# Kernel tuning notes

Hardware: AMD Instinct MI355X
Metric: run time of the kernel (lower is better)

The kernel has to match this reference:

```python
import jax, jax.numpy as jnp
import numpy as np

B, T, C, H = 2, 2048, 1024, 16
D = C // H  # head_dim = 64

def setup_inputs() -> dict:
    key = jax.random.key(0)
    k1, k2, k3 = jax.random.split(key, 3)
    x = jax.random.normal(k1, (B, T, C), dtype=jnp.float32)
    W_qkv = jax.random.normal(k2, (C, 3 * C), dtype=jnp.float32) * (C ** -0.5)
    b_qkv = jnp.zeros((3 * C,), dtype=jnp.float32)
    W_proj = jax.random.normal(k3, (C, C), dtype=jnp.float32) * (C ** -0.5)
    b_proj = jnp.zeros((C,), dtype=jnp.float32)
    return {"x": x, "W_qkv": W_qkv, "b_qkv": b_qkv, "W_proj": W_proj, "b_proj": b_proj}

def reference(x, W_qkv, b_qkv, W_proj, b_proj):
    # qkv projection: [B,T,3C]
    qkv = jnp.einsum('btc,cf->btf', x, W_qkv) + b_qkv
    q, k, v = jnp.split(qkv, 3, axis=-1)
    # split heads -> [B,H,T,D]
    q = q.reshape(B, T, H, D).transpose(0, 2, 1, 3)
    k = k.reshape(B, T, H, D).transpose(0, 2, 1, 3)
    v = v.reshape(B, T, H, D).transpose(0, 2, 1, 3)
    scale = 1.0 / jnp.sqrt(jnp.float32(D))
    att = jnp.einsum('bhqd,bhkd->bhqk', q, k) * scale  # [B,H,T,T]
    causal = jnp.tril(jnp.ones((T, T), dtype=bool))
    att = jnp.where(causal[None, None, :, :], att, jnp.float32(-jnp.inf))
    att = jax.nn.softmax(att, axis=-1)
    y = jnp.einsum('bhqk,bhkd->bhqd', att, v)  # [B,H,T,D]
    y = y.transpose(0, 2, 1, 3).reshape(B, T, C)
    return jnp.einsum('btc,cf->btf', y, W_proj) + b_proj
```

## Files before the change

kernel.cpp:

```cpp
#include <hip/hip_runtime.h>
#include <hip/hip_bf16.h>

#define Bq 2
#define Tq 2048
#define Cq 1024
#define Hq 16
#define Dq 64
#define Mq (Bq * Tq)

typedef __bf16 bf16x8 __attribute__((ext_vector_type(8)));
typedef float f32x4 __attribute__((ext_vector_type(4)));
typedef unsigned uint4v __attribute__((ext_vector_type(4)));
typedef unsigned short u16;

static __device__ __forceinline__ u16 f2bf(float f) {
  union { float f; unsigned u; } v; v.f = f;
  return (u16)((v.u + 0x7fffu + ((v.u >> 16) & 1u)) >> 16);
}

static __device__ __forceinline__ unsigned cvt_pk_bf16(float a, float b) {
  unsigned r;
  asm("v_cvt_pk_bf16_f32 %0, %1, %2" : "=v"(r) : "v"(a), "v"(b));
  return r;
}

static __device__ __forceinline__ f32x4 mfma16(bf16x8 a, bf16x8 b, f32x4 c) {
  return __builtin_amdgcn_mfma_f32_16x16x32_bf16(a, b, c, 0, 0, 0);
}

#define GLD16(g, l)                                                   \
  __builtin_amdgcn_global_load_lds(                                   \
      (const __attribute__((address_space(1))) unsigned int*)(g),     \
      (__attribute__((address_space(3))) unsigned int*)(l), 16, 0, 0)

static __device__ __forceinline__ int swz(int col, int row) {
  return (col & 7) + 8 * (((col >> 3) ^ (row >> 3)) & 7);
}

__global__ __launch_bounds__(256) void convert_x(const float* __restrict__ x,
                                                 u16* __restrict__ xb) {
  int i = (blockIdx.x * 256 + threadIdx.x) * 8;
  float4 a = *(const float4*)(x + i);
  float4 b = *(const float4*)(x + i + 4);
  u16 tmp[8];
  tmp[0] = f2bf(a.x); tmp[1] = f2bf(a.y); tmp[2] = f2bf(a.z); tmp[3] = f2bf(a.w);
  tmp[4] = f2bf(b.x); tmp[5] = f2bf(b.y); tmp[6] = f2bf(b.z); tmp[7] = f2bf(b.w);
  *(uint4*)(xb + i) = *(const uint4*)tmp;
}

__global__ __launch_bounds__(256) void transpose_w(const float* __restrict__ W,
                                                   u16* __restrict__ Wt,
                                                   int K, int N) {
  __shared__ __align__(16) u16 Ts[64][72];
  const int k0 = blockIdx.x * 64, n0 = blockIdx.y * 64;
  const int t = threadIdx.x;
  const int r = t >> 2, c0 = (t & 3) * 16;
  const float* src = W + (size_t)(k0 + r) * N + n0 + c0;
  u16 v16[16];
#pragma unroll
  for (int i = 0; i < 4; i++) {
    float4 f = *(const float4*)(src + 4 * i);
    v16[4 * i + 0] = f2bf(f.x); v16[4 * i + 1] = f2bf(f.y);
    v16[4 * i + 2] = f2bf(f.z); v16[4 * i + 3] = f2bf(f.w);
  }
#pragma unroll
  for (int j = 0; j < 16; j++) Ts[c0 + j][r] = v16[j];
  __syncthreads();
  u16* dst = Wt + (size_t)(n0 + r) * K + k0 + c0;
  *(uint4*)dst = *(const uint4*)&Ts[r][c0];
  *(uint4*)(dst + 8) = *(const uint4*)&Ts[r][c0 + 8];
}

__global__ __launch_bounds__(256) void qkv_gemm(
    const u16* __restrict__ A, const u16* __restrict__ Bt,
    const float* __restrict__ bias,
    u16* __restrict__ qw, u16* __restrict__ kw, u16* __restrict__ vw) {
  const int K = 1024;
  __shared__ __align__(16) u16 As[128][32];
  __shared__ __align__(16) u16 Bs[128][32];
  const int m0 = blockIdx.x * 128, n0 = blockIdx.y * 128;
  const int t = threadIdx.x, lane = t & 63, w = t >> 6;
  const int wm = (w >> 1) * 64, wn = (w & 1) * 64;
  const int l15 = lane & 15, l4 = lane >> 4;
  const int lr = lane >> 2, lc = (lane & 3) * 8;
  f32x4 acc[4][4] = {};
  const u16* ga = A + (size_t)(m0 + w * 16 + lr) * K + lc;
  const u16* gb = Bt + (size_t)(n0 + w * 16 + lr) * K + lc;

  for (int kk = 0; kk < K; kk += 32) {
    __syncthreads();
    GLD16(ga + kk, &As[w * 16][0]);
    GLD16(ga + (size_t)64 * K + kk, &As[64 + w * 16][0]);
    GLD16(gb + kk, &Bs[w * 16][0]);
    GLD16(gb + (size_t)64 * K + kk, &Bs[64 + w * 16][0]);
    __syncthreads();
    bf16x8 af[4], bfr[4];
#pragma unroll
    for (int i = 0; i < 4; i++) {
      af[i] = *(const bf16x8*)&As[wm + i * 16 + l15][l4 * 8];
      bfr[i] = *(const bf16x8*)&Bs[wn + i * 16 + l15][l4 * 8];
    }
#pragma unroll
    for (int mi = 0; mi < 4; mi++)
#pragma unroll
      for (int ni = 0; ni < 4; ni++)
        acc[mi][ni] = mfma16(af[mi], bfr[ni], acc[mi][ni]);
  }
#pragma unroll
  for (int mi = 0; mi < 4; mi++) {
#pragma unroll
    for (int ni = 0; ni < 4; ni++) {
#pragma unroll
      for (int r = 0; r < 4; r++) {
        int row = m0 + wm + mi * 16 + l4 * 4 + r;
        int col = n0 + wn + ni * 16 + l15;
        float val = acc[mi][ni][r] + bias[col];
        int which = col >> 10, c = col & 1023;
        if (which == 0) val *= 0.18033688011112042f;
        int h = c >> 6, d = c & 63;
        int b = row >> 11, tt = row & 2047;
        u16* dst = (which == 0) ? qw : ((which == 1) ? kw : vw);
        dst[(size_t)((b * Hq + h) * Tq + tt) * Dq + d] = f2bf(val);
      }
    }
  }
}

__global__ __launch_bounds__(256, 3) void attn(
    const u16* __restrict__ qw, const u16* __restrict__ kw,
    const u16* __restrict__ vw, u16* __restrict__ yw) {
  const int bh = blockIdx.x;
  const int qy = blockIdx.y;
  const int qb = (qy < 8) ? (15 - qy) : (qy - 8);
  __shared__ __align__(16) u16 Ks[64][72];
  __shared__ __align__(16) u16 Vt[64][72];
  const int t = threadIdx.x, lane = t & 63, w = t >> 6;
  const int l15 = lane & 15, l4 = lane >> 4;
  const size_t base = (size_t)bh * Tq * Dq;
  const int rv = t >> 2, d0 = (t & 3) * 16;

  const int qs0 = qb * 128 + w * 32;
  bf16x8 qf[2][2];
  {
    const u16* qp = qw + base + (size_t)(qs0 + l15) * Dq + l4 * 8;
    qf[0][0] = *(const bf16x8*)qp;
    qf[0][1] = *(const bf16x8*)(qp + 32);
    qf[1][0] = *(const bf16x8*)(qp + 16 * Dq);
    qf[1][1] = *(const bf16x8*)(qp + 16 * Dq + 32);
  }

  float m[2] = {-1e30f, -1e30f}, lsum[2] = {0.f, 0.f};
  f32x4 accO[2][4] = {};
  const int kvmax = 2 * qb + 1;

  const u16* ksrc = kw + base + (size_t)rv * Dq + d0;
  const u16* vsrc = vw + base + (size_t)rv * Dq + d0;
  uint4 kreg0 = *(const uint4*)ksrc, kreg1 = *(const uint4*)(ksrc + 8);
  uint4 vreg0 = *(const uint4*)vsrc, vreg1 = *(const uint4*)(vsrc + 8);

  for (int kv = 0; kv <= kvmax; kv++) {
    __syncthreads();
    *(uint4*)&Ks[rv][d0] = kreg0;
    *(uint4*)&Ks[rv][d0 + 8] = kreg1;
    {
      union { uint4 q[2]; u16 s[16]; } vu;
      vu.q[0] = vreg0; vu.q[1] = vreg1;
#pragma unroll
      for (int jj = 0; jj < 16; jj++) {
        int row = d0 + jj;
        Vt[row][swz(rv, row)] = vu.s[jj];
      }
    }
    if (kv < kvmax) {
      ksrc += 64 * Dq; vsrc += 64 * Dq;
      kreg0 = *(const uint4*)ksrc; kreg1 = *(const uint4*)(ksrc + 8);
      vreg0 = *(const uint4*)vsrc; vreg1 = *(const uint4*)(vsrc + 8);
    }
    __syncthreads();

    if (kv * 64 > qs0 + 31) continue;

    f32x4 sc[2][4];
    __builtin_amdgcn_s_setprio(1);
#pragma unroll
    for (int ct = 0; ct < 4; ct++) {
      bf16x8 kf0 = *(const bf16x8*)&Ks[ct * 16 + l15][l4 * 8];
      bf16x8 kf1 = *(const bf16x8*)&Ks[ct * 16 + l15][32 + l4 * 8];
      f32x4 z0 = {};
      z0 = mfma16(kf0, qf[0][0], z0); z0 = mfma16(kf1, qf[0][1], z0);
      sc[0][ct] = z0;
      f32x4 z1 = {};
      z1 = mfma16(kf0, qf[1][0], z1); z1 = mfma16(kf1, qf[1][1], z1);
      sc[1][ct] = z1;
    }
    __builtin_amdgcn_s_setprio(0);

    if (kv * 64 + 63 > qs0) {
#pragma unroll
      for (int s = 0; s < 2; s++) {
        const int q = qs0 + s * 16 + l15;
#pragma unroll
        for (int ct = 0; ct < 4; ct++)
#pragma unroll
          for (int r = 0; r < 4; r++) {
            int k = kv * 64 + ct * 16 + l4 * 4 + r;
            if (k > q) sc[s][ct][r] = -1e30f;
          }
      }
    }

    bf16x8 pa[2][2];
    const int bsrc = ((lane & 16) << 1) + l15;
#pragma unroll
    for (int s = 0; s < 2; s++) {
      float pmax = sc[s][0][0];
#pragma unroll
      for (int ct = 0; ct < 4; ct++)
#pragma unroll
        for (int r = 0; r < 4; r++) pmax = fmaxf(pmax, sc[s][ct][r]);
      pmax = fmaxf(pmax, __shfl_xor(pmax, 16));
      pmax = fmaxf(pmax, __shfl_xor(pmax, 32));

      if (__any(pmax > m[s] + 8.f)) {
        float mn = fmaxf(m[s], pmax);
        float corr = exp2f(m[s] - mn);
        m[s] = mn;
        lsum[s] *= corr;
#pragma unroll
        for (int r = 0; r < 4; r++) {
          float cb = __shfl(corr, (lane >> 4) * 20 + r);
#pragma unroll
          for (int dt = 0; dt < 4; dt++) accO[s][dt][r] *= cb;
        }
      }

      float psum = 0.f;
#pragma unroll
      for (int ct = 0; ct < 4; ct++)
#pragma unroll
        for (int r = 0; r < 4; r++) {
          float p = exp2f(sc[s][ct][r] - m[s]);
          sc[s][ct][r] = p;
          psum += p;
        }
      psum += __shfl_xor(psum, 16);
      psum += __shfl_xor(psum, 32);
      lsum[s] += psum;

      unsigned pk[4][2];
#pragma unroll
      for (int ct = 0; ct < 4; ct++)
#pragma unroll
        for (int hw = 0; hw < 2; hw++)
          pk[ct][hw] = cvt_pk_bf16(sc[s][ct][2 * hw], sc[s][ct][2 * hw + 1]);
#pragma unroll
      for (int h = 0; h < 2; h++) {
        uint4v pu;
#pragma unroll
        for (int jh = 0; jh < 2; jh++)
#pragma unroll
          for (int hw = 0; hw < 2; hw++) {
            unsigned w0 = __shfl(pk[2 * h][hw], bsrc + 16 * jh);
            unsigned w1 = __shfl(pk[2 * h + 1][hw], bsrc + 16 * jh);
            pu[jh * 2 + hw] = (l4 & 2) ? w1 : w0;
          }
        pa[s][h] = __builtin_bit_cast(bf16x8, pu);
      }
    }

    __builtin_amdgcn_s_setprio(1);
#pragma unroll
    for (int dt = 0; dt < 4; dt++) {
      int Rv = dt * 16 + l15;
      int e = (Rv >> 3) & 7;
      bf16x8 vf0 = *(const bf16x8*)&Vt[Rv][8 * ((l4 ^ e) & 7)];
      bf16x8 vf1 = *(const bf16x8*)&Vt[Rv][8 * (((4 + l4) ^ e) & 7)];
      accO[0][dt] = mfma16(pa[0][0], vf0, accO[0][dt]);
      accO[0][dt] = mfma16(pa[0][1], vf1, accO[0][dt]);
      accO[1][dt] = mfma16(pa[1][0], vf0, accO[1][dt]);
      accO[1][dt] = mfma16(pa[1][1], vf1, accO[1][dt]);
    }
    __builtin_amdgcn_s_setprio(0);
  }

  const int b = bh >> 4, hd = bh & 15;
#pragma unroll
  for (int s = 0; s < 2; s++) {
    float inv = 1.0f / lsum[s];
#pragma unroll
    for (int r = 0; r < 4; r++) {
      float ib = __shfl(inv, (lane >> 4) * 20 + r);
      int tt = qs0 + s * 16 + l4 * 4 + r;
      size_t rowbase = ((size_t)(b * Tq + tt)) * Cq + hd * 64;
#pragma unroll
      for (int dt = 0; dt < 4; dt++)
        yw[rowbase + dt * 16 + l15] = f2bf(accO[s][dt][r] * ib);
    }
  }
}

__global__ __launch_bounds__(256) void proj_gemm(
    const u16* __restrict__ A, const u16* __restrict__ Bt,
    const float* __restrict__ bias, float* __restrict__ out) {
  const int K = 1024, N = 1024;
  __shared__ __align__(16) u16 As[128][32];
  __shared__ __align__(16) u16 Bs[128][32];
  const int m0 = blockIdx.x * 128, n0 = blockIdx.y * 128;
  const int t = threadIdx.x, lane = t & 63, w = t >> 6;
  const int wm = (w >> 1) * 64, wn = (w & 1) * 64;
  const int l15 = lane & 15, l4 = lane >> 4;
  const int lr = lane >> 2, lc = (lane & 3) * 8;
  f32x4 acc[4][4] = {};
  const u16* ga = A + (size_t)(m0 + w * 16 + lr) * K + lc;
  const u16* gb = Bt + (size_t)(n0 + w * 16 + lr) * K + lc;

  for (int kk = 0; kk < K; kk += 32) {
    __syncthreads();
    GLD16(ga + kk, &As[w * 16][0]);
    GLD16(ga + (size_t)64 * K + kk, &As[64 + w * 16][0]);
    GLD16(gb + kk, &Bs[w * 16][0]);
    GLD16(gb + (size_t)64 * K + kk, &Bs[64 + w * 16][0]);
    __syncthreads();
    bf16x8 af[4], bfr[4];
#pragma unroll
    for (int i = 0; i < 4; i++) {
      af[i] = *(const bf16x8*)&As[wm + i * 16 + l15][l4 * 8];
      bfr[i] = *(const bf16x8*)&Bs[wn + i * 16 + l15][l4 * 8];
    }
#pragma unroll
    for (int mi = 0; mi < 4; mi++)
#pragma unroll
      for (int ni = 0; ni < 4; ni++)
        acc[mi][ni] = mfma16(af[mi], bfr[ni], acc[mi][ni]);
  }
#pragma unroll
  for (int mi = 0; mi < 4; mi++) {
#pragma unroll
    for (int ni = 0; ni < 4; ni++) {
#pragma unroll
      for (int r = 0; r < 4; r++) {
        int row = m0 + wm + mi * 16 + l4 * 4 + r;
        int col = n0 + wn + ni * 16 + l15;
        out[(size_t)row * N + col] = acc[mi][ni][r] + bias[col];
      }
    }
  }
}

extern "C" void kernel_launch(void* const* d_in, const int* in_sizes, int n_in,
                              void* d_out, int out_size, void* d_ws, size_t ws_size,
                              hipStream_t stream) {
  const float* x = (const float*)d_in[0];
  const float* W_qkv = (const float*)d_in[1];
  const float* b_qkv = (const float*)d_in[2];
  const float* W_proj = (const float*)d_in[3];
  const float* b_proj = (const float*)d_in[4];
  float* out = (float*)d_out;

  const size_t qkv_elems = (size_t)Bq * Hq * Tq * Dq;
  u16* qw = (u16*)d_ws;
  u16* kw = qw + qkv_elems;
  u16* vw = kw + qkv_elems;
  u16* xb = vw + qkv_elems;
  u16* wt = xb + (size_t)Mq * Cq;

  convert_x<<<dim3((Mq * Cq) / (256 * 8)), 256, 0, stream>>>(x, xb);
  transpose_w<<<dim3(Cq / 64, 3 * Cq / 64), 256, 0, stream>>>(W_qkv, wt, Cq, 3 * Cq);
  qkv_gemm<<<dim3(Mq / 128, 3 * Cq / 128), 256, 0, stream>>>(xb, wt, b_qkv, qw, kw, vw);
  transpose_w<<<dim3(Cq / 64, Cq / 64), 256, 0, stream>>>(W_proj, wt, Cq, Cq);
  u16* yw = xb;
  attn<<<dim3(Bq * Hq, Tq / 128), 256, 0, stream>>>(qw, kw, vw, yw);
  proj_gemm<<<dim3(Mq / 128, Cq / 128), 256, 0, stream>>>(yw, wt, b_proj, out);
}
```

Baseline: 203.7 us.

## Pre-transpose V and double-buffer K/V via async global-to-LDS loads in attention

Adds a separate kernel that transposes V into a [D,T] layout with a permuted key order, so the attention kernel can stream K and V tiles straight into LDS using global_load_lds. It also double-buffers those tiles to overlap the next tile's load with the current tile's compute, which cuts one barrier per iteration. The permuted key order lets the P fragments be packed directly from registers without cross-lane shuffles. In exchange it adds an extra kernel launch plus a round trip of V through memory, doubles LDS use, and lowers the launch-bounds occupancy hint from 3 to 2.

```diff
diff --git a/kernel.cpp b/kernel.cpp
--- a/kernel.cpp
+++ b/kernel.cpp
@@ -33,8 +33,8 @@
       (const __attribute__((address_space(1))) unsigned int*)(g),     \
       (__attribute__((address_space(3))) unsigned int*)(l), 16, 0, 0)
 
-static __device__ __forceinline__ int swz(int col, int row) {
-  return (col & 7) + 8 * (((col >> 3) ^ (row >> 3)) & 7);
+static __device__ __forceinline__ int sperm(int k) {
+  return (k & 0x23) | ((k & 0x0C) << 1) | ((k & 0x10) >> 2);
 }
 
 __global__ __launch_bounds__(256) void convert_x(const float* __restrict__ x,
@@ -69,6 +69,26 @@
   u16* dst = Wt + (size_t)(n0 + r) * K + k0 + c0;
   *(uint4*)dst = *(const uint4*)&Ts[r][c0];
   *(uint4*)(dst + 8) = *(const uint4*)&Ts[r][c0 + 8];
+}
+
+__global__ __launch_bounds__(256) void transpose_v(const u16* __restrict__ vw,
+                                                   u16* __restrict__ vts) {
+  __shared__ __align__(16) u16 Ts[64][72];
+  const int tile = blockIdx.x, bh = blockIdx.y;
+  const size_t base = (size_t)bh * Tq * Dq;
+  const int t = threadIdx.x;
+  const int rv = t >> 2, c0 = (t & 3) * 16;
+  const u16* src = vw + base + (size_t)(tile * 64 + rv) * Dq + c0;
+  union { uint4 q[2]; u16 s[16]; } vu;
+  vu.q[0] = *(const uint4*)src;
+  vu.q[1] = *(const uint4*)(src + 8);
+  const int sc = sperm(rv);
+#pragma unroll
+  for (int j = 0; j < 16; j++) Ts[c0 + j][sc] = vu.s[j];
+  __syncthreads();
+  u16* dst = vts + base + (size_t)rv * Tq + tile * 64 + c0;
+  *(uint4*)dst = *(const uint4*)&Ts[rv][c0];
+  *(uint4*)(dst + 8) = *(const uint4*)&Ts[rv][c0 + 8];
 }
 
 __global__ __launch_bounds__(256) void qkv_gemm(
@@ -106,6 +126,9 @@
       for (int ni = 0; ni < 4; ni++)
         acc[mi][ni] = mfma16(af[mi], bfr[ni], acc[mi][ni]);
   }
+  const int which = n0 >> 10;
+  u16* dst = (which == 0) ? qw : ((which == 1) ? kw : vw);
+  const float qsc = (which == 0) ? 0.18033688011112042f : 1.0f;
 #pragma unroll
   for (int mi = 0; mi < 4; mi++) {
 #pragma unroll
@@ -114,32 +137,29 @@
       for (int r = 0; r < 4; r++) {
         int row = m0 + wm + mi * 16 + l4 * 4 + r;
         int col = n0 + wn + ni * 16 + l15;
-        float val = acc[mi][ni][r] + bias[col];
-        int which = col >> 10, c = col & 1023;
-        if (which == 0) val *= 0.18033688011112042f;
+        float val = (acc[mi][ni][r] + bias[col]) * qsc;
+        int c = col & 1023;
         int h = c >> 6, d = c & 63;
         int b = row >> 11, tt = row & 2047;
-        u16* dst = (which == 0) ? qw : ((which == 1) ? kw : vw);
         dst[(size_t)((b * Hq + h) * Tq + tt) * Dq + d] = f2bf(val);
       }
     }
   }
 }
 
-__global__ __launch_bounds__(256, 3) void attn(
+__global__ __launch_bounds__(256, 2) void attn(
     const u16* __restrict__ qw, const u16* __restrict__ kw,
-    const u16* __restrict__ vw, u16* __restrict__ yw) {
+    const u16* __restrict__ vts, u16* __restrict__ yw) {
   const int bh = blockIdx.x;
   const int qy = blockIdx.y;
   const int qb = (qy < 8) ? (15 - qy) : (qy - 8);
-  __shared__ __align__(16) u16 Ks[64][72];
-  __shared__ __align__(16) u16 Vt[64][72];
+  __shared__ __align__(16) u16 Ks[2][64][64];
+  __shared__ __align__(16) u16 Vt[2][64][64];
   const int t = threadIdx.x, lane = t & 63, w = t >> 6;
   const int l15 = lane & 15, l4 = lane >> 4;
   const size_t base = (size_t)bh * Tq * Dq;
-  const int rv = t >> 2, d0 = (t & 3) * 16;
-
   const int qs0 = qb * 128 + w * 32;
+
   bf16x8 qf[2][2];
   {
     const u16* qp = qw + base + (size_t)(qs0 + l15) * Dq + l4 * 8;
@@ -149,139 +169,127 @@
     qf[1][1] = *(const bf16x8*)(qp + 16 * Dq + 32);
   }
 
+  const int r0 = w * 8 + (lane >> 3);
+  const int c0 = ((lane & 7) ^ (r0 & 7)) * 8;
+  const u16* kbase = kw + base;
+  const u16* vbase = vts + base;
+
+#define STAGE(kv_, b_)                                                      \
+  do {                                                                      \
+    GLD16(kbase + (size_t)((kv_)*64 + r0) * Dq + c0, &Ks[b_][w * 8][0]);    \
+    GLD16(kbase + (size_t)((kv_)*64 + 32 + r0) * Dq + c0,                   \
+          &Ks[b_][32 + w * 8][0]);                                          \
+    GLD16(vbase + (size_t)r0 * Tq + (kv_)*64 + c0, &Vt[b_][w * 8][0]);      \
+    GLD16(vbase + (size_t)(32 + r0) * Tq + (kv_)*64 + c0,                   \
+          &Vt[b_][32 + w * 8][0]);                                          \
+  } while (0)
+
   float m[2] = {-1e30f, -1e30f}, lsum[2] = {0.f, 0.f};
   f32x4 accO[2][4] = {};
   const int kvmax = 2 * qb + 1;
 
-  const u16* ksrc = kw + base + (size_t)rv * Dq + d0;
-  const u16* vsrc = vw + base + (size_t)rv * Dq + d0;
-  uint4 kreg0 = *(const uint4*)ksrc, kreg1 = *(const uint4*)(ksrc + 8);
-  uint4 vreg0 = *(const uint4*)vsrc, vreg1 = *(const uint4*)(vsrc + 8);
+  STAGE(0, 0);
+  __syncthreads();
 
   for (int kv = 0; kv <= kvmax; kv++) {
-    __syncthreads();
-    *(uint4*)&Ks[rv][d0] = kreg0;
-    *(uint4*)&Ks[rv][d0 + 8] = kreg1;
-    {
-      union { uint4 q[2]; u16 s[16]; } vu;
-      vu.q[0] = vreg0; vu.q[1] = vreg1;
-#pragma unroll
-      for (int jj = 0; jj < 16; jj++) {
-        int row = d0 + jj;
-        Vt[row][swz(rv, row)] = vu.s[jj];
-      }
-    }
-    if (kv < kvmax) {
-      ksrc += 64 * Dq; vsrc += 64 * Dq;
-      kreg0 = *(const uint4*)ksrc; kreg1 = *(const uint4*)(ksrc + 8);
-      vreg0 = *(const uint4*)vsrc; vreg1 = *(const uint4*)(vsrc + 8);
-    }
-    __syncthreads();
-
-    if (kv * 64 > qs0 + 31) continue;
-
-    f32x4 sc[2][4];
-    __builtin_amdgcn_s_setprio(1);
-#pragma unroll
-    for (int ct = 0; ct < 4; ct++) {
-      bf16x8 kf0 = *(const bf16x8*)&Ks[ct * 16 + l15][l4 * 8];
-      bf16x8 kf1 = *(const bf16x8*)&Ks[ct * 16 + l15][32 + l4 * 8];
-      f32x4 z0 = {};
-      z0 = mfma16(kf0, qf[0][0], z0); z0 = mfma16(kf1, qf[0][1], z0);
-      sc[0][ct] = z0;
-      f32x4 z1 = {};
-      z1 = mfma16(kf0, qf[1][0], z1); z1 = mfma16(kf1, qf[1][1], z1);
-      sc[1][ct] = z1;
-    }
-    __builtin_amdgcn_s_setprio(0);
-
-    if (kv * 64 + 63 > qs0) {
+    const int cur = kv & 1;
+    if (kv < kvmax) STAGE(kv + 1, cur ^ 1);
+
+    if (kv * 64 <= qs0 + 31) {
+      f32x4 sc[2][4];
+      __builtin_amdgcn_s_setprio(1);
+#pragma unroll
+      for (int ct = 0; ct < 4; ct++) {
+        const int kr = ct * 16 + l15, e = l15 & 7;
+        bf16x8 kf0 = *(const bf16x8*)&Ks[cur][kr][8 * (l4 ^ e)];
+        bf16x8 kf1 = *(const bf16x8*)&Ks[cur][kr][8 * ((4 + l4) ^ e)];
+        f32x4 z0 = {};
+        z0 = mfma16(kf0, qf[0][0], z0); z0 = mfma16(kf1, qf[0][1], z0);
+        sc[0][ct] = z0;
+        f32x4 z1 = {};
+        z1 = mfma16(kf0, qf[1][0], z1); z1 = mfma16(kf1, qf[1][1], z1);
+        sc[1][ct] = z1;
+      }
+      __builtin_amdgcn_s_setprio(0);
+
+      if (kv * 64 + 63 > qs0) {
+#pragma unroll
+        for (int s = 0; s < 2; s++) {
+          const int q = qs0 + s * 16 + l15;
+#pragma unroll
+          for (int ct = 0; ct < 4; ct++)
+#pragma unroll
+            for (int r = 0; r < 4; r++) {
+              int k = kv * 64 + ct * 16 + l4 * 4 + r;
+              if (k > q) sc[s][ct][r] = -1e30f;
+            }
+        }
+      }
+
+      bf16x8 pa[2][2];
 #pragma unroll
       for (int s = 0; s < 2; s++) {
-        const int q = qs0 + s * 16 + l15;
+        float pmax = sc[s][0][0];
 #pragma unroll
         for (int ct = 0; ct < 4; ct++)
 #pragma unroll
+          for (int r = 0; r < 4; r++) pmax = fmaxf(pmax, sc[s][ct][r]);
+        pmax = fmaxf(pmax, __shfl_xor(pmax, 16));
+        pmax = fmaxf(pmax, __shfl_xor(pmax, 32));
+
+        if (__any(pmax > m[s] + 8.f)) {
+          float mn = fmaxf(m[s], pmax);
+          float corr = exp2f(m[s] - mn);
+          m[s] = mn;
+          lsum[s] *= corr;
+#pragma unroll
           for (int r = 0; r < 4; r++) {
-            int k = kv * 64 + ct * 16 + l4 * 4 + r;
-            if (k > q) sc[s][ct][r] = -1e30f;
+            float cb = __shfl(corr, (lane >> 4) * 20 + r);
+#pragma unroll
+            for (int dt = 0; dt < 4; dt++) accO[s][dt][r] *= cb;
           }
-      }
-    }
-
-    bf16x8 pa[2][2];
-    const int bsrc = ((lane & 16) << 1) + l15;
-#pragma unroll
-    for (int s = 0; s < 2; s++) {
-      float pmax = sc[s][0][0];
-#pragma unroll
-      for (int ct = 0; ct < 4; ct++)
-#pragma unroll
-        for (int r = 0; r < 4; r++) pmax = fmaxf(pmax, sc[s][ct][r]);
-      pmax = fmaxf(pmax, __shfl_xor(pmax, 16));
-      pmax = fmaxf(pmax, __shfl_xor(pmax, 32));
-
-      if (__any(pmax > m[s] + 8.f)) {
-        float mn = fmaxf(m[s], pmax);
-        float corr = exp2f(m[s] - mn);
-        m[s] = mn;
-        lsum[s] *= corr;
-#pragma unroll
-        for (int r = 0; r < 4; r++) {
-          float cb = __shfl(corr, (lane >> 4) * 20 + r);
-#pragma unroll
-          for (int dt = 0; dt < 4; dt++) accO[s][dt][r] *= cb;
         }
-      }
-
-      float psum = 0.f;
-#pragma unroll
-      for (int ct = 0; ct < 4; ct++)
-#pragma unroll
-        for (int r = 0; r < 4; r++) {
-          float p = exp2f(sc[s][ct][r] - m[s]);
-          sc[s][ct][r] = p;
-          psum += p;
+
+        float psum = 0.f;
+#pragma unroll
+        for (int ct = 0; ct < 4; ct++)
+#pragma unroll
+          for (int r = 0; r < 4; r++) {
+            float p = exp2f(sc[s][ct][r] - m[s]);
+            sc[s][ct][r] = p;
+            psum += p;
+          }
+        psum += __shfl_xor(psum, 16);
+        psum += __shfl_xor(psum, 32);
+        lsum[s] += psum;
+
+#pragma unroll
+        for (int h = 0; h < 2; h++) {
+          uint4v pu;
+          pu[0] = cvt_pk_bf16(sc[s][2 * h][0], sc[s][2 * h][1]);
+          pu[1] = cvt_pk_bf16(sc[s][2 * h][2], sc[s][2 * h][3]);
+          pu[2] = cvt_pk_bf16(sc[s][2 * h + 1][0], sc[s][2 * h + 1][1]);
+          pu[3] = cvt_pk_bf16(sc[s][2 * h + 1][2], sc[s][2 * h + 1][3]);
+          pa[s][h] = __builtin_bit_cast(bf16x8, pu);
         }
-      psum += __shfl_xor(psum, 16);
-      psum += __shfl_xor(psum, 32);
-      lsum[s] += psum;
-
-      unsigned pk[4][2];
-#pragma unroll
-      for (int ct = 0; ct < 4; ct++)
-#pragma unroll
-        for (int hw = 0; hw < 2; hw++)
-          pk[ct][hw] = cvt_pk_bf16(sc[s][ct][2 * hw], sc[s][ct][2 * hw + 1]);
-#pragma unroll
-      for (int h = 0; h < 2; h++) {
-        uint4v pu;
-#pragma unroll
-        for (int jh = 0; jh < 2; jh++)
-#pragma unroll
-          for (int hw = 0; hw < 2; hw++) {
-            unsigned w0 = __shfl(pk[2 * h][hw], bsrc + 16 * jh);
-            unsigned w1 = __shfl(pk[2 * h + 1][hw], bsrc + 16 * jh);
-            pu[jh * 2 + hw] = (l4 & 2) ? w1 : w0;
-          }
-        pa[s][h] = __builtin_bit_cast(bf16x8, pu);
-      }
-    }
-
-    __builtin_amdgcn_s_setprio(1);
-#pragma unroll
-    for (int dt = 0; dt < 4; dt++) {
-      int Rv = dt * 16 + l15;
-      int e = (Rv >> 3) & 7;
-      bf16x8 vf0 = *(const bf16x8*)&Vt[Rv][8 * ((l4 ^ e) & 7)];
-      bf16x8 vf1 = *(const bf16x8*)&Vt[Rv][8 * (((4 + l4) ^ e) & 7)];
-      accO[0][dt] = mfma16(pa[0][0], vf0, accO[0][dt]);
-      accO[0][dt] = mfma16(pa[0][1], vf1, accO[0][dt]);
-      accO[1][dt] = mfma16(pa[1][0], vf0, accO[1][dt]);
-      accO[1][dt] = mfma16(pa[1][1], vf1, accO[1][dt]);
-    }
-    __builtin_amdgcn_s_setprio(0);
-  }
+      }
+
+      __builtin_amdgcn_s_setprio(1);
+#pragma unroll
+      for (int dt = 0; dt < 4; dt++) {
+        const int Rv = dt * 16 + l15, e = l15 & 7;
+        bf16x8 vf0 = *(const bf16x8*)&Vt[cur][Rv][8 * (l4 ^ e)];
+        bf16x8 vf1 = *(const bf16x8*)&Vt[cur][Rv][8 * ((4 + l4) ^ e)];
+        accO[0][dt] = mfma16(pa[0][0], vf0, accO[0][dt]);
+        accO[0][dt] = mfma16(pa[0][1], vf1, accO[0][dt]);
+        accO[1][dt] = mfma16(pa[1][0], vf0, accO[1][dt]);
+        accO[1][dt] = mfma16(pa[1][1], vf1, accO[1][dt]);
+      }
+      __builtin_amdgcn_s_setprio(0);
+    }
+    __syncthreads();
+  }
+#undef STAGE
 
   const int b = bh >> 4, hd = bh & 15;
 #pragma unroll
@@ -363,12 +371,14 @@
   u16* vw = kw + qkv_elems;
   u16* xb = vw + qkv_elems;
   u16* wt = xb + (size_t)Mq * Cq;
+  u16* vts = xb;
+  u16* yw = vw;
 
   convert_x<<<dim3((Mq * Cq) / (256 * 8)), 256, 0, stream>>>(x, xb);
   transpose_w<<<dim3(Cq / 64, 3 * Cq / 64), 256, 0, stream>>>(W_qkv, wt, Cq, 3 * Cq);
   qkv_gemm<<<dim3(Mq / 128, 3 * Cq / 128), 256, 0, stream>>>(xb, wt, b_qkv, qw, kw, vw);
+  transpose_v<<<dim3(Tq / 64, Bq * Hq), 256, 0, stream>>>(vw, vts);
   transpose_w<<<dim3(Cq / 64, Cq / 64), 256, 0, stream>>>(W_proj, wt, Cq, Cq);
-  u16* yw = xb;
-  attn<<<dim3(Bq * Hq, Tq / 128), 256, 0, stream>>>(qw, kw, vw, yw);
+  attn<<<dim3(Bq * Hq, Tq / 128), 256, 0, stream>>>(qw, kw, vts, yw);
   proj_gemm<<<dim3(Mq / 128, Cq / 128), 256, 0, stream>>>(yw, wt, b_proj, out);
 }
```

Measured after the change: 219.3 us. 1.08x slower.
